# Optimization experiments

Hardware: AMD Instinct MI355X
Metric: run time of the kernel (lower is better)

## Reference

```python
import jax, jax.numpy as jnp
import numpy as np

TEMP = 0.05          # args.temp_lp_loss
NUM_CLASSES = 256

def _l2norm(x):
    return x / jnp.linalg.norm(x, axis=-1, keepdims=True)

def setup_inputs() -> dict:
    key = jax.random.key(0)
    k1, k2, k3 = jax.random.split(key, 3)
    B, C, Bs, TOPK = 2048, 2048, 4096, 4
    feats = _l2norm(jax.random.normal(k1, (B, C), jnp.float32))
    feats_s = _l2norm(jax.random.normal(k2, (Bs, TOPK, C), jnp.float32))
    labels = jax.random.randint(k3, (B,), 0, NUM_CLASSES, dtype=jnp.int32)
    # every class 0..255 appears, so each query has >=1 positive support
    labels_s = jnp.arange(Bs * TOPK, dtype=jnp.int32) % NUM_CLASSES
    return {"feats": feats, "feats_s": feats_s, "labels": labels, "labels_s": labels_s}

def reference(feats, feats_s, labels, labels_s):
    Bs, topk, C = feats_s.shape
    fs = feats_s.reshape(Bs * topk, C)                    # [N, C]
    E = jnp.exp(jnp.einsum('bc,nc->bn', feats, fs) / TEMP)  # [B, N]
    is_pos = labels[:, None] == labels_s[None, :]          # [B, N]
    # per-row hardest positive (min over positives of exp-sim)
    pos_min = jnp.min(jnp.where(is_pos, E, jnp.inf), axis=1)   # [B]
    # sum over all negatives of exp-sim
    neg_sum = jnp.sum(jnp.where(is_pos, 0.0, E), axis=1)       # [B]
    loss = -jnp.log(pos_min / (pos_min + neg_sum + 1e-6) + 1e-6)
    return jnp.mean(loss)
```

## Files before the change

kernel.cpp:

```cpp
#include <hip/hip_runtime.h>
#include <stdint.h>

#define M_TOTAL 2048
#define N_TOTAL 16384
#define K_TOTAL 2048
#define NPARTS  256
#define NT      (K_TOTAL / 128)

#define SCALE_E8M0 0x76767676
#define SCALE_F 512.0f

typedef __attribute__((ext_vector_type(4))) int   int4v;
typedef __attribute__((ext_vector_type(8))) int   int8v;
typedef __attribute__((ext_vector_type(4))) float floatx4;

__device__ __forceinline__ uint32_t pack8(float4 v) {
    int p = __builtin_amdgcn_cvt_pk_fp8_f32(v.x * SCALE_F, v.y * SCALE_F, 0, 0);
    p = __builtin_amdgcn_cvt_pk_fp8_f32(v.z * SCALE_F, v.w * SCALE_F, p, 1);
    return (uint32_t)p;
}

__device__ __forceinline__ void cvt_loop16(const float4* __restrict__ src,
                                           uint4* __restrict__ dst,
                                           int i, int stride, int n16) {
    for (; i < n16; i += stride) {
        const float4* p = src + (size_t)i * 4;
        uint4 o;
        o.x = pack8(p[0]);
        o.y = pack8(p[1]);
        o.z = pack8(p[2]);
        o.w = pack8(p[3]);
        dst[i] = o;
    }
}

__global__ __launch_bounds__(256) void cvt_fp8_all(
        const float4* __restrict__ a, const float4* __restrict__ b,
        uint4* __restrict__ oa, uint4* __restrict__ ob) {
    if (blockIdx.x < 512)
        cvt_loop16(a, oa, blockIdx.x * 256 + threadIdx.x, 512 * 256,
                   M_TOTAL * K_TOTAL / 16);
    else
        cvt_loop16(b, ob, (blockIdx.x - 512) * 256 + threadIdx.x, 2048 * 256,
                   N_TOTAL * K_TOTAL / 16);
}

__device__ __forceinline__ void load16(const void* g, void* l) {
    __builtin_amdgcn_global_load_lds(
        (const __attribute__((address_space(1))) void*)g,
        (__attribute__((address_space(3))) void*)l, 16, 0, 0);
}

__global__ __launch_bounds__(512, 2) void gemm_lp(
        const char* __restrict__ Af8, const char* __restrict__ Bf8,
        const int* __restrict__ labels, const int* __restrict__ labels_s,
        float* __restrict__ pminp, float* __restrict__ psump) {
    __shared__ __align__(16) char smA[2][256][128];
    __shared__ __align__(16) char smB[2][256][128];
    __shared__ int lab_m[256];
    __shared__ int lab_n[256];

    const int t    = threadIdx.x;
    const int lane = t & 63;
    const int wave = t >> 6;
    const int wm   = wave >> 2;
    const int wn   = wave & 3;
    const int m0   = blockIdx.y * 256;
    const int n0   = blockIdx.x * 256;

    if (t < 256) lab_m[t] = labels[m0 + t];
    else         lab_n[t - 256] = labels_s[n0 + t - 256];

    const int rq = t >> 3;
    const int qt = (t & 7) ^ ((t >> 3) & 7);
    const char* aG = Af8 + (long)(m0 + rq) * K_TOTAL + qt * 16;
    const char* bG = Bf8 + (long)(n0 + rq) * K_TOTAL + qt * 16;
    const int ldst = wave * 1024;

#define STAGE_A(T, J) load16(aG + (J) * 64 * K_TOTAL + (T) * 128, \
                             &smA[(T) & 1][(J) * 64][0] + ldst)
#define STAGE_B(T, J) load16(bG + (J) * 64 * K_TOTAL + (T) * 128, \
                             &smB[(T) & 1][(J) * 64][0] + ldst)

    const int quad = lane >> 4;
    const int lcol = lane & 15;
    const int plo = ((2 * quad)     ^ (lcol & 7)) << 4;
    const int phi = ((2 * quad + 1) ^ (lcol & 7)) << 4;
    const char* aF = &smA[0][wm * 128 + lcol][0];
    const char* bF = &smB[0][wn * 64  + lcol][0];

    floatx4 acc[8][4];
#pragma unroll
    for (int mi = 0; mi < 8; ++mi)
#pragma unroll
        for (int ni = 0; ni < 4; ++ni)
            acc[mi][ni] = (floatx4){0.f, 0.f, 0.f, 0.f};

#pragma unroll
    for (int j = 0; j < 4; ++j) { STAGE_A(0, j); STAGE_B(0, j); }
    STAGE_A(1, 0); STAGE_B(1, 0);
    STAGE_A(1, 1); STAGE_B(1, 1);
    asm volatile("s_waitcnt vmcnt(4) lgkmcnt(0)" ::: "memory");
    __builtin_amdgcn_s_barrier();

#pragma unroll 1
    for (int kt = 0; kt < NT; ++kt) {
        const char* aB = aF + (kt & 1) * 32768;
        const char* bB = bF + (kt & 1) * 32768;

        if (kt + 1 < NT) {
            STAGE_A(kt + 1, 2); STAGE_B(kt + 1, 2);
            STAGE_A(kt + 1, 3); STAGE_B(kt + 1, 3);
        }

        int8v bv[4];
#pragma unroll
        for (int ni = 0; ni < 4; ++ni) {
            int4v lo = *(const int4v*)(bB + ni * 2048 + plo);
            int4v hi = *(const int4v*)(bB + ni * 2048 + phi);
            bv[ni] = (int8v){lo.x, lo.y, lo.z, lo.w, hi.x, hi.y, hi.z, hi.w};
        }
        __builtin_amdgcn_s_setprio(1);
#pragma unroll
        for (int mi = 0; mi < 8; ++mi) {
            int4v lo = *(const int4v*)(aB + mi * 2048 + plo);
            int4v hi = *(const int4v*)(aB + mi * 2048 + phi);
            int8v av = (int8v){lo.x, lo.y, lo.z, lo.w, hi.x, hi.y, hi.z, hi.w};
#pragma unroll
            for (int ni = 0; ni < 4; ++ni)
                acc[mi][ni] = __builtin_amdgcn_mfma_scale_f32_16x16x128_f8f6f4(
                    av, bv[ni], acc[mi][ni],
                    0, 0,
                    0, SCALE_E8M0,
                    0, SCALE_E8M0);
        }
        __builtin_amdgcn_s_setprio(0);

        if (kt + 1 < NT) {
            asm volatile("s_waitcnt lgkmcnt(0)" ::: "memory");
            __builtin_amdgcn_s_barrier();
            if (kt + 2 < NT) {
                STAGE_A(kt + 2, 0); STAGE_B(kt + 2, 0);
                STAGE_A(kt + 2, 1); STAGE_B(kt + 2, 1);
                asm volatile("s_waitcnt vmcnt(4)" ::: "memory");
            } else {
                asm volatile("s_waitcnt vmcnt(0)" ::: "memory");
            }
            __builtin_amdgcn_s_barrier();
        }
    }
#undef STAGE_A
#undef STAGE_B

    const float scale = 28.853900817779268f;
#pragma unroll
    for (int mi = 0; mi < 8; ++mi) {
#pragma unroll
        for (int r = 0; r < 4; ++r) {
            const int row_local = wm * 128 + mi * 16 + quad * 4 + r;
            const int lab = lab_m[row_local];
            float minv = __builtin_inff();
            float sumv = 0.f;
#pragma unroll
            for (int ni = 0; ni < 4; ++ni) {
                const int col_local = wn * 64 + ni * 16 + lcol;
                const float e = exp2f(acc[mi][ni][r] * scale);
                const bool pos = (lab_n[col_local] == lab);
                minv = pos ? fminf(minv, e) : minv;
                sumv = pos ? sumv : (sumv + e);
            }
#pragma unroll
            for (int off = 1; off < 16; off <<= 1) {
                minv = fminf(minv, __shfl_xor(minv, off, 16));
                sumv += __shfl_xor(sumv, off, 16);
            }
            if (lcol == 0) {
                const long idx = (long)(m0 + row_local) * NPARTS + blockIdx.x * 4 + wn;
                pminp[idx] = minv;
                psump[idx] = sumv;
            }
        }
    }
}

__global__ __launch_bounds__(256) void reduce_rows(
        const float* __restrict__ pminp, const float* __restrict__ psump,
        float* __restrict__ loss) {
    const int row  = blockIdx.x * 4 + (threadIdx.x >> 6);
    const int lane = threadIdx.x & 63;
    float m = __builtin_inff();
    float s = 0.f;
#pragma unroll
    for (int k = 0; k < NPARTS / 64; ++k) {
        const long j = (long)row * NPARTS + lane + k * 64;
        m = fminf(m, pminp[j]);
        s += psump[j];
    }
#pragma unroll
    for (int off = 1; off < 64; off <<= 1) {
        m = fminf(m, __shfl_xor(m, off, 64));
        s += __shfl_xor(s, off, 64);
    }
    if (lane == 0) loss[row] = -logf(m / (m + s + 1e-6f) + 1e-6f);
}

__global__ void final_mean(const float* __restrict__ loss, float* __restrict__ out) {
    float s = 0.f;
    for (int i = threadIdx.x; i < M_TOTAL; i += 256) s += loss[i];
#pragma unroll
    for (int off = 32; off > 0; off >>= 1) s += __shfl_xor(s, off, 64);
    __shared__ float wsum[4];
    if ((threadIdx.x & 63) == 0) wsum[threadIdx.x >> 6] = s;
    __syncthreads();
    if (threadIdx.x == 0)
        out[0] = (wsum[0] + wsum[1] + wsum[2] + wsum[3]) * (1.0f / (float)M_TOTAL);
}

extern "C" void kernel_launch(void* const* d_in, const int* in_sizes, int n_in,
                              void* d_out, int out_size, void* d_ws, size_t ws_size,
                              hipStream_t stream) {
    const float* feats    = (const float*)d_in[0];
    const float* feats_s  = (const float*)d_in[1];
    const int*   labels   = (const int*)d_in[2];
    const int*   labels_s = (const int*)d_in[3];
    float*       out      = (float*)d_out;

    char* ws = (char*)d_ws;
    char*  Af8   = ws;
    char*  Bf8   = ws + 4194304;
    float* pminp = (float*)(ws + 37748736);
    float* psump = (float*)(ws + 39845888);
    float* loss  = (float*)(ws + 41943040);

    cvt_fp8_all<<<2560, 256, 0, stream>>>((const float4*)feats, (const float4*)feats_s,
                                          (uint4*)Af8, (uint4*)Bf8);

    dim3 grid(N_TOTAL / 256, M_TOTAL / 256);
    gemm_lp<<<grid, 512, 0, stream>>>(Af8, Bf8, labels, labels_s, pminp, psump);

    reduce_rows<<<512, 256, 0, stream>>>(pminp, psump, loss);
    final_mean<<<1, 256, 0, stream>>>(loss, out);
}
```

Before: 303.8 us.

## Restructure fp8 GEMM main loop into ping-pong staged LDS reads and MFMA phases

Rewrites the K loop of the fp8 MFMA GEMM. All global-to-LDS loads for the next tile are issued at once. A-fragment reads are interleaved in pairs with MFMA groups, separated by barriers, sched_barriers and partial lgkmcnt waits. The B fragments for the next tile are prefetched into a second register set, and the loop is unrolled by two to swap the bv/bn buffers. The aim is to overlap LDS reads with MFMA issue and coordinate waves across the CU. In exchange it adds more barriers, higher register pressure and a full vmcnt(0) wait each tile.

```diff
diff --git a/kernel.cpp b/kernel.cpp
--- a/kernel.cpp
+++ b/kernel.cpp
@@ -51,6 +51,12 @@
         (__attribute__((address_space(3))) void*)l, 16, 0, 0);
 }
 
+__device__ __forceinline__ int8v frag8(const char* lo_p, const char* hi_p) {
+    int4v lo = *(const int4v*)lo_p;
+    int4v hi = *(const int4v*)hi_p;
+    return (int8v){lo.x, lo.y, lo.z, lo.w, hi.x, hi.y, hi.z, hi.w};
+}
+
 __global__ __launch_bounds__(512, 2) void gemm_lp(
         const char* __restrict__ Af8, const char* __restrict__ Bf8,
         const int* __restrict__ labels, const int* __restrict__ labels_s,
@@ -77,9 +83,9 @@
     const char* bG = Bf8 + (long)(n0 + rq) * K_TOTAL + qt * 16;
     const int ldst = wave * 1024;
 
-#define STAGE_A(T, J) load16(aG + (J) * 64 * K_TOTAL + (T) * 128, \
+#define STAGE_A(T, J) load16(aG + (T) * 128 + (J) * 64 * K_TOTAL, \
                              &smA[(T) & 1][(J) * 64][0] + ldst)
-#define STAGE_B(T, J) load16(bG + (J) * 64 * K_TOTAL + (T) * 128, \
+#define STAGE_B(T, J) load16(bG + (T) * 128 + (J) * 64 * K_TOTAL, \
                              &smB[(T) & 1][(J) * 64][0] + ldst)
 
     const int quad = lane >> 4;
@@ -89,6 +95,8 @@
     const char* aF = &smA[0][wm * 128 + lcol][0];
     const char* bF = &smB[0][wn * 64  + lcol][0];
 
+#define RD(P) frag8((P) + plo, (P) + phi)
+
     floatx4 acc[8][4];
 #pragma unroll
     for (int mi = 0; mi < 8; ++mi)
@@ -96,59 +104,87 @@
         for (int ni = 0; ni < 4; ++ni)
             acc[mi][ni] = (floatx4){0.f, 0.f, 0.f, 0.f};
 
+    int8v bv[4], bn[4];
+
+#define MFMA_PAIR(R, AV0, AV1, BARR)                                           \
+    do {                                                                       \
+        _Pragma("unroll")                                                      \
+        for (int ni = 0; ni < 4; ++ni) {                                       \
+            acc[R][ni] = __builtin_amdgcn_mfma_scale_f32_16x16x128_f8f6f4(     \
+                AV0, BARR[ni], acc[R][ni], 0, 0, 0, SCALE_E8M0, 0, SCALE_E8M0);\
+            acc[R + 1][ni] = __builtin_amdgcn_mfma_scale_f32_16x16x128_f8f6f4( \
+                AV1, BARR[ni], acc[R + 1][ni], 0, 0, 0, SCALE_E8M0, 0,         \
+                SCALE_E8M0);                                                   \
+        }                                                                      \
+    } while (0)
+
+#define TILE(KT, BC, BN)                                                       \
+    do {                                                                       \
+        const int cur_ = (KT) & 1;                                             \
+        const char* aB_ = aF + cur_ * 32768;                                   \
+        const char* bN_ = bF + (cur_ ^ 1) * 32768;                             \
+                             \
+        if ((KT) + 1 < NT) {                                                   \
+            _Pragma("unroll")                                                  \
+            for (int j = 0; j < 4; ++j) {                                      \
+                STAGE_A((KT) + 1, j);                                          \
+                STAGE_B((KT) + 1, j);                                          \
+            }                                                                  \
+        }                                                                      \
+        int8v a0_ = RD(aB_ + 0 * 2048), a1_ = RD(aB_ + 1 * 2048);              \
+        int8v a2_ = RD(aB_ + 2 * 2048), a3_ = RD(aB_ + 3 * 2048);              \
+        __builtin_amdgcn_s_barrier();                                          \
+        asm volatile("s_waitcnt lgkmcnt(4)" ::: "memory");                     \
+        __builtin_amdgcn_sched_barrier(0);                                     \
+        __builtin_amdgcn_s_setprio(1);                                         \
+        MFMA_PAIR(0, a0_, a1_, BC);                                            \
+        __builtin_amdgcn_s_setprio(0);                                         \
+        __builtin_amdgcn_s_barrier();                                          \
+                                                                  \
+        int8v a4_ = RD(aB_ + 4 * 2048), a5_ = RD(aB_ + 5 * 2048);              \
+        __builtin_amdgcn_s_barrier();                                          \
+        asm volatile("s_waitcnt lgkmcnt(4)" ::: "memory");                     \
+        __builtin_amdgcn_sched_barrier(0);                                     \
+        __builtin_amdgcn_s_setprio(1);                                         \
+        MFMA_PAIR(2, a2_, a3_, BC);                                            \
+        __builtin_amdgcn_s_setprio(0);                                         \
+        __builtin_amdgcn_s_barrier();                                          \
+                                                                  \
+        int8v a6_ = RD(aB_ + 6 * 2048), a7_ = RD(aB_ + 7 * 2048);              \
+        __builtin_amdgcn_s_barrier();                                          \
+        asm volatile("s_waitcnt lgkmcnt(4)" ::: "memory");                     \
+        __builtin_amdgcn_sched_barrier(0);                                     \
+        __builtin_amdgcn_s_setprio(1);                                         \
+        MFMA_PAIR(4, a4_, a5_, BC);                                            \
+        __builtin_amdgcn_s_setprio(0);                                         \
+        asm volatile("s_waitcnt vmcnt(0)" ::: "memory");                       \
+        __builtin_amdgcn_s_barrier();                \
+                          \
+        _Pragma("unroll")                                                      \
+        for (int ni = 0; ni < 4; ++ni) BN[ni] = RD(bN_ + ni * 2048);           \
+        asm volatile("s_waitcnt lgkmcnt(8)" ::: "memory");                     \
+        __builtin_amdgcn_sched_barrier(0);                                     \
+        __builtin_amdgcn_s_setprio(1);                                         \
+        MFMA_PAIR(6, a6_, a7_, BC);                                            \
+        __builtin_amdgcn_s_setprio(0);                                         \
+        __builtin_amdgcn_s_barrier();  \
+    } while (0)
+
 #pragma unroll
     for (int j = 0; j < 4; ++j) { STAGE_A(0, j); STAGE_B(0, j); }
-    STAGE_A(1, 0); STAGE_B(1, 0);
-    STAGE_A(1, 1); STAGE_B(1, 1);
-    asm volatile("s_waitcnt vmcnt(4) lgkmcnt(0)" ::: "memory");
+    asm volatile("s_waitcnt vmcnt(0)" ::: "memory");
     __builtin_amdgcn_s_barrier();
+#pragma unroll
+    for (int ni = 0; ni < 4; ++ni) bv[ni] = RD(bF + ni * 2048);
 
 #pragma unroll 1
-    for (int kt = 0; kt < NT; ++kt) {
-        const char* aB = aF + (kt & 1) * 32768;
-        const char* bB = bF + (kt & 1) * 32768;
-
-        if (kt + 1 < NT) {
-            STAGE_A(kt + 1, 2); STAGE_B(kt + 1, 2);
-            STAGE_A(kt + 1, 3); STAGE_B(kt + 1, 3);
-        }
-
-        int8v bv[4];
-#pragma unroll
-        for (int ni = 0; ni < 4; ++ni) {
-            int4v lo = *(const int4v*)(bB + ni * 2048 + plo);
-            int4v hi = *(const int4v*)(bB + ni * 2048 + phi);
-            bv[ni] = (int8v){lo.x, lo.y, lo.z, lo.w, hi.x, hi.y, hi.z, hi.w};
-        }
-        __builtin_amdgcn_s_setprio(1);
-#pragma unroll
-        for (int mi = 0; mi < 8; ++mi) {
-            int4v lo = *(const int4v*)(aB + mi * 2048 + plo);
-            int4v hi = *(const int4v*)(aB + mi * 2048 + phi);
-            int8v av = (int8v){lo.x, lo.y, lo.z, lo.w, hi.x, hi.y, hi.z, hi.w};
-#pragma unroll
-            for (int ni = 0; ni < 4; ++ni)
-                acc[mi][ni] = __builtin_amdgcn_mfma_scale_f32_16x16x128_f8f6f4(
-                    av, bv[ni], acc[mi][ni],
-                    0, 0,
-                    0, SCALE_E8M0,
-                    0, SCALE_E8M0);
-        }
-        __builtin_amdgcn_s_setprio(0);
-
-        if (kt + 1 < NT) {
-            asm volatile("s_waitcnt lgkmcnt(0)" ::: "memory");
-            __builtin_amdgcn_s_barrier();
-            if (kt + 2 < NT) {
-                STAGE_A(kt + 2, 0); STAGE_B(kt + 2, 0);
-                STAGE_A(kt + 2, 1); STAGE_B(kt + 2, 1);
-                asm volatile("s_waitcnt vmcnt(4)" ::: "memory");
-            } else {
-                asm volatile("s_waitcnt vmcnt(0)" ::: "memory");
-            }
-            __builtin_amdgcn_s_barrier();
-        }
-    }
+    for (int kt = 0; kt < NT; kt += 2) {
+        TILE(kt, bv, bn);
+        TILE(kt + 1, bn, bv);
+    }
+#undef TILE
+#undef MFMA_PAIR
+#undef RD
 #undef STAGE_A
 #undef STAGE_B
 
```

New measurement: 334.0 us. 1.1x slower.

## Split GEMM k-step into four phases interleaving LDS reads, global loads, MFMA

Applied to the files above, without the earlier changes.

Restructures the main GEMM loop into four phases. Each phase reads a pair of A fragments, issues one quarter of the next tile's global-to-LDS loads, and runs eight MFMAs between barriers, in the style of a ping-pong schedule. The intent is to spread memory traffic evenly across the compute and keep the two co-resident workgroups alternating between memory and MFMA work. The cost is more barriers per k-step, and the staging order of the tile halves changes, which moves the wait points.

```diff
diff --git a/kernel.cpp b/kernel.cpp
--- a/kernel.cpp
+++ b/kernel.cpp
@@ -51,6 +51,12 @@
         (__attribute__((address_space(3))) void*)l, 16, 0, 0);
 }
 
+__device__ __forceinline__ int8v frag8(const char* lo_p, const char* hi_p) {
+    int4v lo = *(const int4v*)lo_p;
+    int4v hi = *(const int4v*)hi_p;
+    return (int8v){lo.x, lo.y, lo.z, lo.w, hi.x, hi.y, hi.z, hi.w};
+}
+
 __global__ __launch_bounds__(512, 2) void gemm_lp(
         const char* __restrict__ Af8, const char* __restrict__ Bf8,
         const int* __restrict__ labels, const int* __restrict__ labels_s,
@@ -77,10 +83,15 @@
     const char* bG = Bf8 + (long)(n0 + rq) * K_TOTAL + qt * 16;
     const int ldst = wave * 1024;
 
-#define STAGE_A(T, J) load16(aG + (J) * 64 * K_TOTAL + (T) * 128, \
+#define STAGE_A(T, J) load16(aG + (T) * 128 + (J) * 64 * K_TOTAL, \
                              &smA[(T) & 1][(J) * 64][0] + ldst)
-#define STAGE_B(T, J) load16(bG + (J) * 64 * K_TOTAL + (T) * 128, \
+#define STAGE_B(T, J) load16(bG + (T) * 128 + (J) * 64 * K_TOTAL, \
                              &smB[(T) & 1][(J) * 64][0] + ldst)
+#define STAGE_H(T, H)                                                          \
+    do {                                                                       \
+        if ((H) < 2) { STAGE_A(T, (H) * 2); STAGE_A(T, (H) * 2 + 1); }         \
+        else { STAGE_B(T, ((H) - 2) * 2); STAGE_B(T, ((H) - 2) * 2 + 1); }     \
+    } while (0)
 
     const int quad = lane >> 4;
     const int lcol = lane & 15;
@@ -89,6 +100,8 @@
     const char* aF = &smA[0][wm * 128 + lcol][0];
     const char* bF = &smB[0][wn * 64  + lcol][0];
 
+#define RD(P) frag8((P) + plo, (P) + phi)
+
     floatx4 acc[8][4];
 #pragma unroll
     for (int mi = 0; mi < 8; ++mi)
@@ -96,59 +109,71 @@
         for (int ni = 0; ni < 4; ++ni)
             acc[mi][ni] = (floatx4){0.f, 0.f, 0.f, 0.f};
 
-#pragma unroll
-    for (int j = 0; j < 4; ++j) { STAGE_A(0, j); STAGE_B(0, j); }
-    STAGE_A(1, 0); STAGE_B(1, 0);
-    STAGE_A(1, 1); STAGE_B(1, 1);
-    asm volatile("s_waitcnt vmcnt(4) lgkmcnt(0)" ::: "memory");
+    int8v bv[4];
+
+#define MFMA_PAIR(R, AV0, AV1)                                                 \
+    do {                                                                       \
+        _Pragma("unroll")                                                      \
+        for (int ni = 0; ni < 4; ++ni) {                                       \
+            acc[R][ni] = __builtin_amdgcn_mfma_scale_f32_16x16x128_f8f6f4(     \
+                AV0, bv[ni], acc[R][ni], 0, 0, 0, SCALE_E8M0, 0, SCALE_E8M0);  \
+            acc[R + 1][ni] = __builtin_amdgcn_mfma_scale_f32_16x16x128_f8f6f4( \
+                AV1, bv[ni], acc[R + 1][ni], 0, 0, 0, SCALE_E8M0, 0,           \
+                SCALE_E8M0);                                                   \
+        }                                                                      \
+    } while (0)
+
+#define PHASE_TAIL(R, AV0, AV1)                                                \
+    __builtin_amdgcn_s_barrier();                                              \
+    asm volatile("s_waitcnt lgkmcnt(0)" ::: "memory");                         \
+    __builtin_amdgcn_s_setprio(1);                                             \
+    MFMA_PAIR(R, AV0, AV1);                                                    \
+    __builtin_amdgcn_s_setprio(0);                                             \
     __builtin_amdgcn_s_barrier();
 
+    STAGE_H(0, 0); STAGE_H(0, 1); STAGE_H(0, 2); STAGE_H(0, 3);
+    STAGE_H(1, 0);
+    asm volatile("s_waitcnt vmcnt(2)" ::: "memory");
+    __builtin_amdgcn_s_barrier();
+
 #pragma unroll 1
-    for (int kt = 0; kt < NT; ++kt) {
-        const char* aB = aF + (kt & 1) * 32768;
-        const char* bB = bF + (kt & 1) * 32768;
-
-        if (kt + 1 < NT) {
-            STAGE_A(kt + 1, 2); STAGE_B(kt + 1, 2);
-            STAGE_A(kt + 1, 3); STAGE_B(kt + 1, 3);
-        }
-
-        int8v bv[4];
-#pragma unroll
-        for (int ni = 0; ni < 4; ++ni) {
-            int4v lo = *(const int4v*)(bB + ni * 2048 + plo);
-            int4v hi = *(const int4v*)(bB + ni * 2048 + phi);
-            bv[ni] = (int8v){lo.x, lo.y, lo.z, lo.w, hi.x, hi.y, hi.z, hi.w};
-        }
-        __builtin_amdgcn_s_setprio(1);
-#pragma unroll
-        for (int mi = 0; mi < 8; ++mi) {
-            int4v lo = *(const int4v*)(aB + mi * 2048 + plo);
-            int4v hi = *(const int4v*)(aB + mi * 2048 + phi);
-            int8v av = (int8v){lo.x, lo.y, lo.z, lo.w, hi.x, hi.y, hi.z, hi.w};
-#pragma unroll
-            for (int ni = 0; ni < 4; ++ni)
-                acc[mi][ni] = __builtin_amdgcn_mfma_scale_f32_16x16x128_f8f6f4(
-                    av, bv[ni], acc[mi][ni],
-                    0, 0,
-                    0, SCALE_E8M0,
-                    0, SCALE_E8M0);
-        }
-        __builtin_amdgcn_s_setprio(0);
-
-        if (kt + 1 < NT) {
-            asm volatile("s_waitcnt lgkmcnt(0)" ::: "memory");
+    for (int T = 0; T < NT; ++T) {
+        const char* aB = aF + (T & 1) * 32768;
+        const char* bB = bF + (T & 1) * 32768;
+        const bool s1 = (T + 1 < NT);
+
+        bv[0] = RD(bB + 0 * 2048);
+        bv[1] = RD(bB + 1 * 2048);
+        bv[2] = RD(bB + 2 * 2048);
+        bv[3] = RD(bB + 3 * 2048);
+        int8v a0 = RD(aB + 0 * 2048), a1 = RD(aB + 1 * 2048);
+        if (s1) STAGE_H(T + 1, 1);
+        PHASE_TAIL(0, a0, a1)
+
+        int8v a2 = RD(aB + 2 * 2048), a3 = RD(aB + 3 * 2048);
+        if (s1) STAGE_H(T + 1, 2);
+        PHASE_TAIL(2, a2, a3)
+
+        int8v a4 = RD(aB + 4 * 2048), a5 = RD(aB + 5 * 2048);
+        if (s1) STAGE_H(T + 1, 3);
+        PHASE_TAIL(4, a4, a5)
+
+        int8v a6 = RD(aB + 6 * 2048), a7 = RD(aB + 7 * 2048);
+        PHASE_TAIL(6, a6, a7)
+
+        if (T + 2 < NT) {
+            STAGE_H(T + 2, 0);
+            asm volatile("s_waitcnt vmcnt(2)" ::: "memory");
             __builtin_amdgcn_s_barrier();
-            if (kt + 2 < NT) {
-                STAGE_A(kt + 2, 0); STAGE_B(kt + 2, 0);
-                STAGE_A(kt + 2, 1); STAGE_B(kt + 2, 1);
-                asm volatile("s_waitcnt vmcnt(4)" ::: "memory");
-            } else {
-                asm volatile("s_waitcnt vmcnt(0)" ::: "memory");
-            }
+        } else if (T + 1 < NT) {
+            asm volatile("s_waitcnt vmcnt(0)" ::: "memory");
             __builtin_amdgcn_s_barrier();
         }
     }
+#undef PHASE_TAIL
+#undef MFMA_PAIR
+#undef RD
+#undef STAGE_H
 #undef STAGE_A
 #undef STAGE_B
 
```

Result: slower. 313.6 us (+3.2%).
